# Kernel optimization log

Measured on AMD Instinct MI355X. Metric: run time of the kernel, lower is better.

## Reference

```python
import jax, jax.numpy as jnp
import numpy as np
from jax import lax

B, T_IN, T_OUT = 32, 384, 400
N_MEL, ENC, ATT_RNN, DEC_RNN, PRENET, ATT_DIM = 80, 512, 1024, 1024, 256, 128
LOC_F, LOC_K = 32, 31
NEG = -1e9  # stand-in for -inf score_mask_value (safe for softmax grad)


def setup_inputs() -> dict:
    key = jax.random.key(0)
    ks = jax.random.split(key, 20)
    g = lambda i, shape, s=0.02: jax.random.normal(ks[i], shape, dtype=jnp.float32) * s
    return {
        "memory": jax.random.normal(ks[0], (B, T_IN, ENC), dtype=jnp.float32),
        "decoder_inputs": jax.random.normal(ks[1], (B, N_MEL, T_OUT), dtype=jnp.float32),
        "memory_lengths": jax.random.randint(ks[2], (B,), T_IN // 2, T_IN + 1, dtype=jnp.int32),
        "prenet_w1": g(3, (PRENET, N_MEL)),
        "prenet_w2": g(4, (PRENET, PRENET)),
        "att_rnn_wih": g(5, (4 * ATT_RNN, PRENET + ENC)),
        "att_rnn_whh": g(6, (4 * ATT_RNN, ATT_RNN)),
        "att_rnn_bih": jnp.zeros((4 * ATT_RNN,), jnp.float32),
        "att_rnn_bhh": jnp.zeros((4 * ATT_RNN,), jnp.float32),
        "query_w": g(7, (ATT_DIM, ATT_RNN)),
        "memory_w": g(8, (ATT_DIM, ENC)),
        "v_w": g(9, (1, ATT_DIM)),
        "loc_conv_w": g(10, (LOC_F, 2, LOC_K)),
        "loc_dense_w": g(11, (ATT_DIM, LOC_F)),
        "dec_rnn_wih": g(12, (4 * DEC_RNN, ATT_RNN + ENC)),
        "dec_rnn_whh": g(13, (4 * DEC_RNN, DEC_RNN)),
        "dec_rnn_bih": jnp.zeros((4 * DEC_RNN,), jnp.float32),
        "dec_rnn_bhh": jnp.zeros((4 * DEC_RNN,), jnp.float32),
        "proj_w": g(14, (N_MEL, DEC_RNN + ENC)),
        "proj_b": jnp.zeros((N_MEL,), jnp.float32),
        "gate_w": g(15, (1, DEC_RNN + ENC)),
        "gate_b": jnp.zeros((1,), jnp.float32),
    }


def _lstm_cell(x, h, c, wih, whh, bih, bhh):
    gates = x @ wih.T + bih + h @ whh.T + bhh
    i, f, g, o = jnp.split(gates, 4, axis=-1)
    c2 = jax.nn.sigmoid(f) * c + jax.nn.sigmoid(i) * jnp.tanh(g)
    return jax.nn.sigmoid(o) * jnp.tanh(c2), c2


def reference(memory, decoder_inputs, memory_lengths, prenet_w1, prenet_w2,
              att_rnn_wih, att_rnn_whh, att_rnn_bih, att_rnn_bhh,
              query_w, memory_w, v_w, loc_conv_w, loc_dense_w,
              dec_rnn_wih, dec_rnn_whh, dec_rnn_bih, dec_rnn_bhh,
              proj_w, proj_b, gate_w, gate_b):
    pad = (LOC_K - 1) // 2
    pad_mask = jnp.arange(T_IN)[None, :] >= memory_lengths[:, None]  # (B, T_in), True = padded
    processed_memory = jnp.einsum('bte,ae->bta', memory, memory_w)  # (B, T_in, A)

    # parse_decoder_inputs + go frame: (T_out+1, B, n_mel)
    dec_in = jnp.concatenate([jnp.zeros((1, B, N_MEL), memory.dtype),
                              jnp.transpose(decoder_inputs, (2, 0, 1))], axis=0)
    # Prenet on whole teacher-forced sequence (eval: no dropout)
    pre = jax.nn.relu(jnp.einsum('tbm,pm->tbp', dec_in, prenet_w1))
    pre = jax.nn.relu(jnp.einsum('tbp,qp->tbq', pre, prenet_w2))  # (T_out+1, B, prenet)
    xs = pre[:-1]  # T_out decode steps

    def step(carry, x):
        ah, ac, dh, dc, aw, awc, ctx = carry
        # attention RNN
        ah, ac = _lstm_cell(jnp.concatenate([x, ctx], -1), ah, ac,
                            att_rnn_wih, att_rnn_whh, att_rnn_bih, att_rnn_bhh)
        # location-sensitive additive attention
        pq = (ah @ query_w.T)[:, None, :]  # (B, 1, A)
        cat = jnp.stack([aw, awc], axis=1)  # (B, 2, T_in)
        loc = lax.conv_general_dilated(cat, loc_conv_w, (1,), [(pad, pad)],
                                       dimension_numbers=('NCH', 'OIH', 'NCH'))  # (B, F, T_in)
        ploc = jnp.einsum('bft,af->bta', loc, loc_dense_w)  # (B, T_in, A)
        e = jnp.squeeze(jnp.tanh(pq + ploc + processed_memory) @ v_w.T, -1)  # (B, T_in)
        e = jnp.where(pad_mask, NEG, e)
        w = jax.nn.softmax(e, axis=1)
        ctx = jnp.einsum('bt,bte->be', w, memory)  # (B, enc)
        awc = awc + w
        # decoder RNN
        dh, dc = _lstm_cell(jnp.concatenate([ah, ctx], -1), dh, dc,
                            dec_rnn_wih, dec_rnn_whh, dec_rnn_bih, dec_rnn_bhh)
        hc = jnp.concatenate([dh, ctx], -1)  # (B, dec+enc)
        mel = hc @ proj_w.T + proj_b  # (B, n_mel)
        gate = hc @ gate_w.T + gate_b  # (B, 1)
        return (ah, ac, dh, dc, w, awc, ctx), (mel, gate, w)

    z = lambda d: jnp.zeros((B, d), memory.dtype)
    carry0 = (z(ATT_RNN), z(ATT_RNN), z(DEC_RNN), z(DEC_RNN),
              jnp.zeros((B, T_IN), memory.dtype), jnp.zeros((B, T_IN), memory.dtype), z(ENC))
    _, (mels, gates, aligns) = lax.scan(step, carry0, xs)
    mel_outputs = jnp.transpose(mels, (1, 2, 0))  # (B, n_mel, T_out)
    gate_outputs = jnp.transpose(jnp.squeeze(gates, -1), (1, 0))  # (B, T_out)
    alignments = jnp.transpose(aligns, (1, 0, 2))  # (B, T_out, T_in)
    return mel_outputs, gate_outputs, alignments
```

## Files before the change

kernel.cpp:

```cpp
#include <hip/hip_runtime.h>

typedef _Float16 h16;
typedef _Float16 half8 __attribute__((ext_vector_type(8)));
typedef float f32x4 __attribute__((ext_vector_type(4)));

#define NEGV -1000000000.0f
#define MFMA16(a,b,c) __builtin_amdgcn_mfma_f32_16x16x32_f16(a,b,c,0,0,0)

struct Params {
  const float *memory, *dec_in; const int *memlen;
  const float *w1, *w2;
  const float *awih, *awhh, *abih, *abhh;
  const float *qw, *mw, *vw, *lcw, *ldw;
  const float *dwih, *dwhh, *dbih, *dbhh;
  const float *pw, *pb, *gw, *gb;
  float *out, *ws;
};

constexpr long long XALLF_H = 0;
constexpr long long PMH_H   = 3276800;
constexpr long long PLB_H   = 4849664;
constexpr long long AWIHF_H = 6422528;
constexpr long long AWHHF_H = 9568256;
constexpr long long DWIHF_H = 13762560;
constexpr long long DWHHF_H = 20054016;
constexpr long long LCWF_H  = 24248320;
constexpr long long LDWF_H  = 24250368;
constexpr long long AHF_H   = 24254464;
constexpr long long DHF_H   = 24320000;
constexpr long long CTXF_H  = 24352768;
constexpr long long MEMF_H  = 24812544;
constexpr long long PWF_H   = 31104000;
constexpr long long QWF_H   = 31226880;
constexpr long long ZERO_F0 = 12127232;
constexpr long long AC_F    = 12184576;
constexpr long long DC_F    = 12217344;
constexpr long long AW_F    = 12250112;
constexpr long long AWC_F   = 12262400;
constexpr long long DPART_F = 12274688;
constexpr long long BAR_F   = 12405760;
constexpr int  ZERO_LEN = 278528;
constexpr unsigned NBLK = 512;
constexpr long long GATE0  = 1024000;
constexpr long long ALIGN0 = 1036800;

union SMem {
  float pmstage[12][512];
  struct { float x[5][80]; float l1[5][256]; } pre;
  struct { float red[16][2][16][17]; } g;
  struct { float awseg[2][128]; h16 im2[96][72]; h16 locT[96][32];
           unsigned p16[96][64]; } ploc;
  struct { float ah[1024]; float pq[128]; float pqp[8][128]; float vv[128];
           float e[384]; float w[384]; float red[32];
           float ctxred[4][256][2]; } row;
  struct { float hc[1536]; float mp[80][8]; float gacc; } mel;
};

__device__ __forceinline__ float sigf(float x){ return 1.0f/(1.0f+__expf(-x)); }
__device__ __forceinline__ float tanhfast(float x){ float e2 = __expf(2.0f*x); return 1.0f - 2.0f/(e2+1.0f); }

__device__ __forceinline__ float aldf(const float* p){
  return __hip_atomic_load(p, __ATOMIC_RELAXED, __HIP_MEMORY_SCOPE_AGENT);
}
__device__ __forceinline__ void astf(float* p, float v){
  __hip_atomic_store(p, v, __ATOMIC_RELAXED, __HIP_MEMORY_SCOPE_AGENT);
}
__device__ __forceinline__ unsigned long long aldu64(const h16* p){
  return __hip_atomic_load((const unsigned long long*)p, __ATOMIC_RELAXED, __HIP_MEMORY_SCOPE_AGENT);
}
__device__ __forceinline__ half8 ald16(const h16* p){
  union { unsigned long long q[2]; half8 v; } u;
  u.q[0] = __hip_atomic_load((const unsigned long long*)p,     __ATOMIC_RELAXED, __HIP_MEMORY_SCOPE_AGENT);
  u.q[1] = __hip_atomic_load(((const unsigned long long*)p)+1, __ATOMIC_RELAXED, __HIP_MEMORY_SCOPE_AGENT);
  return u.v;
}
__device__ __forceinline__ void asth(h16* p, float v){
  union { h16 h; unsigned short s; } u; u.h = (h16)v;
  __hip_atomic_store((unsigned short*)p, u.s, __ATOMIC_RELAXED, __HIP_MEMORY_SCOPE_AGENT);
}
__device__ __forceinline__ void astu32(unsigned* p, unsigned v){
  __hip_atomic_store(p, v, __ATOMIC_RELAXED, __HIP_MEMORY_SCOPE_AGENT);
}

__device__ __forceinline__ void gbar(unsigned* cnts, unsigned ep, bool full){
  __syncthreads();
  if (threadIdx.x == 0){
    if (full) __threadfence();
    __hip_atomic_fetch_add(&cnts[(blockIdx.x & 7)*64], 1u, __ATOMIC_RELEASE, __HIP_MEMORY_SCOPE_AGENT);
    const unsigned tgt = ep*NBLK;
    for (;;){
      unsigned s = 0;
      #pragma unroll
      for (int i = 0; i < 8; ++i)
        s += __hip_atomic_load(&cnts[i*64], __ATOMIC_RELAXED, __HIP_MEMORY_SCOPE_AGENT);
      if (s >= tgt) break;
      __builtin_amdgcn_s_sleep(4);
    }
    if (full) __threadfence();
  }
  __syncthreads();
}

__global__ void init_kernel(float* ws){
  unsigned* c = (unsigned*)(ws + BAR_F);
  if (threadIdx.x < 512) c[threadIdx.x] = 0u;
}

__global__ __launch_bounds__(1024, 8)
void decoder_kernel(Params P){
  __shared__ SMem sm;
  const int tid = threadIdx.x;
  const int bid = blockIdx.x;
  float* ws = P.ws;
  h16*   wsh = (h16*)ws;
  unsigned* bar = (unsigned*)(ws + BAR_F);
  unsigned ep = 0;

  const int lane = tid & 63, wv = tid >> 6;
  const int i16 = lane & 15, q = lane >> 4;

  {
    const long long gtid = (long long)bid*1024 + tid;
    const long long GS = 524288;
    for (long long i = gtid; i < ZERO_LEN; i += GS) ws[ZERO_F0 + i] = 0.f;
    for (long long i = gtid; i < 3145728; i += GS) wsh[AWIHF_H+i] = (h16)P.awih[i];
    for (long long i = gtid; i < 4194304; i += GS) wsh[AWHHF_H+i] = (h16)P.awhh[i];
    for (long long i = gtid; i < 6291456; i += GS) wsh[DWIHF_H+i] = (h16)P.dwih[i];
    for (long long i = gtid; i < 4194304; i += GS) wsh[DWHHF_H+i] = (h16)P.dwhh[i];
    for (long long i = gtid; i < 6291456; i += GS) wsh[MEMF_H+i] = (h16)P.memory[i];
    for (long long i = gtid; i < 122880; i += GS) wsh[PWF_H+i] = (h16)P.pw[i];
    for (long long i = gtid; i < 131072; i += GS) wsh[QWF_H+i] = (h16)P.qw[i];
    for (long long i = gtid; i < 2048; i += GS){
      int f = (int)(i >> 6), kk = (int)(i & 63), ch = kk >> 5, k = kk & 31;
      wsh[LCWF_H+i] = (k < 31) ? (h16)P.lcw[f*62 + ch*31 + k] : (h16)0.f;
    }
    for (long long i = gtid; i < 4096; i += GS) wsh[LDWF_H+i] = (h16)P.ldw[i];
  }
  {
    const int b = bid >> 4, part = bid & 15;
    for (int sub = 0; sub < 2; ++sub){
      const int t0 = part*24 + sub*12;
      __syncthreads();
      for (int i = tid; i < 1536; i += 1024){
        int row = i >> 7, c4 = (i & 127) << 2;
        *reinterpret_cast<float4*>(&sm.pmstage[row][c4]) =
          *reinterpret_cast<const float4*>(P.memory + ((long long)(b*384 + t0 + row))*512 + c4);
      }
      __syncthreads();
      if (tid < 512){
        const int a = tid & 127, th = tid >> 7;
        float acc[3] = {0,0,0};
        const float* mwr = P.mw + (long long)a*512;
        for (int e = 0; e < 512; ++e){
          float wvv = mwr[e];
          #pragma unroll
          for (int jj = 0; jj < 3; ++jj) acc[jj] += wvv*sm.pmstage[th*3+jj][e];
        }
        #pragma unroll
        for (int jj = 0; jj < 3; ++jj)
          wsh[PMH_H + ((long long)b*128 + a)*384 + t0 + th*3 + jj] = (h16)acc[jj];
      }
    }
  }
  {
    for (int batch = 0; batch < 5; ++batch){
      const int pbase = bid*25 + batch*5;
      __syncthreads();
      for (int i = tid; i < 400; i += 1024){
        int j = i/80, m = i%80;
        int p = pbase + j; int tq = p >> 5, bb = p & 31;
        float v = 0.f;
        if (tq > 0) v = P.dec_in[((long long)bb*80 + m)*400 + (tq-1)];
        sm.pre.x[j][m] = v;
      }
      __syncthreads();
      {
        float acc[5] = {0,0,0,0,0};
        if (tid < 256){
          const float* w1r = P.w1 + (long long)tid*80;
          for (int m = 0; m < 80; ++m){
            float wvv = w1r[m];
            #pragma unroll
            for (int j = 0; j < 5; ++j) acc[j] += wvv*sm.pre.x[j][m];
          }
        }
        __syncthreads();
        if (tid < 256){
          #pragma unroll
          for (int j = 0; j < 5; ++j) sm.pre.l1[j][tid] = fmaxf(acc[j], 0.f);
        }
      }
      __syncthreads();
      if (tid < 256){
        float acc[5] = {0,0,0,0,0};
        const float* w2r = P.w2 + (long long)tid*256;
        for (int pp = 0; pp < 256; ++pp){
          float wvv = w2r[pp];
          #pragma unroll
          for (int j = 0; j < 5; ++j) acc[j] += wvv*sm.pre.l1[j][pp];
        }
        #pragma unroll
        for (int j = 0; j < 5; ++j){
          int p = pbase + j; int tq = p >> 5, bb = p & 31;
          wsh[XALLF_H + ((long long)tq*32 + bb)*256 + tid] = (h16)fmaxf(acc[j], 0.f);
        }
      }
    }
  }
  gbar(bar, ++ep, true);

  for (int t = 0; t <= 400; ++t){
    const int cur = t & 1, prv = (t+1) & 1;

    if (bid < 256){
      if (t < 400){
        const int u0 = bid*4;
        const int n = ((i16 >> 2)*1024) + u0 + (i16 & 3);
        f32x4 acc0 = {0,0,0,0}, acc1 = {0,0,0,0};
        const long long prvO = (long long)prv*32768;
        const int s0 = (wv*56) >> 4, s1 = ((wv+1)*56) >> 4;
        for (int s = s0; s < s1; ++s){
          const int k0 = s*32;
          const h16* pA = (k0 < 768) ? wsh + AWIHF_H + (long long)n*768 + k0 + q*8
                                     : wsh + AWHHF_H + (long long)n*1024 + (k0-768) + q*8;
          half8 A = *(const half8*)pA;
          half8 B0, B1;
          if (k0 < 256){
            B0 = *(const half8*)(wsh + XALLF_H + ((long long)t*32 + i16)*256 + k0 + q*8);
            B1 = *(const half8*)(wsh + XALLF_H + ((long long)t*32 + 16 + i16)*256 + k0 + q*8);
          } else if (k0 < 768){
            B0 = ald16(wsh + CTXF_H + i16*512 + (k0-256) + q*8);
            B1 = ald16(wsh + CTXF_H + (16+i16)*512 + (k0-256) + q*8);
          } else {
            B0 = ald16(wsh + AHF_H + prvO + i16*1024 + (k0-768) + q*8);
            B1 = ald16(wsh + AHF_H + prvO + (16+i16)*1024 + (k0-768) + q*8);
          }
          acc0 = MFMA16(A, B0, acc0);
          acc1 = MFMA16(A, B1, acc1);
        }
        #pragma unroll
        for (int r = 0; r < 4; ++r){
          sm.g.red[wv][0][q*4+r][i16] = acc0[r];
          sm.g.red[wv][1][q*4+r][i16] = acc1[r];
        }
        __syncthreads();
        if (tid < 128){
          const int uu = tid >> 5, b = tid & 31;
          const int bt2 = b >> 4, c = b & 15;
          float g4[4];
          #pragma unroll
          for (int g = 0; g < 4; ++g){
            const int tr = g*4 + uu;
            float v = 0.f;
            #pragma unroll
            for (int w = 0; w < 16; ++w) v += sm.g.red[w][bt2][tr][c];
            const int ng = g*1024 + u0 + uu;
            g4[g] = v + P.abih[ng] + P.abhh[ng];
          }
          const long long idx = (long long)b*1024 + u0 + uu;
          float c2 = sigf(g4[1])*ws[AC_F + idx] + sigf(g4[0])*tanhfast(g4[2]);
          ws[AC_F + idx] = c2;
          asth(wsh + AHF_H + (long long)cur*32768 + idx, sigf(g4[3])*tanhfast(c2));
        }
      }
    } else if (bid < 384){
      if (t < 400){
        const int pb = bid - 256, b = pb >> 2, tbase = (pb & 3)*96;
        for (int i = tid; i < 252; i += 1024){
          int ch = i / 126, ix = i % 126;
          int pos = tbase - 15 + ix;
          float v = 0.f;
          if (pos >= 0 && pos < 384)
            v = aldf(ws + (ch ? AWC_F : AW_F) + b*384 + pos);
          sm.ploc.awseg[ch][ix] = v;
        }
        __syncthreads();
        for (int i = tid; i < 96*64; i += 1024){
          int tt = i >> 6, kk = i & 63, ch = kk >> 5, k = kk & 31;
          sm.ploc.im2[tt][kk] = (k < 31) ? (h16)sm.ploc.awseg[ch][tt + k] : (h16)0.f;
        }
        __syncthreads();
        {
          int tile = wv;
          if (tile < 12){
            int tT = tile % 6, tF = tile / 6;
            f32x4 a = {0,0,0,0};
            #pragma unroll
            for (int ks = 0; ks < 2; ++ks){
              half8 A = *(const half8*)&sm.ploc.im2[tT*16 + i16][ks*32 + q*8];
              half8 B = *(const half8*)(wsh + LCWF_H + (tF*16 + i16)*64 + ks*32 + q*8);
              a = MFMA16(A, B, a);
            }
            #pragma unroll
            for (int r = 0; r < 4; ++r)
              sm.ploc.locT[tT*16 + q*4 + r][tF*16 + i16] = (h16)a[r];
          }
        }
        __syncthreads();
        unsigned short* s16 = (unsigned short*)&sm.ploc.p16[0][0];
        #pragma unroll
        for (int p = 0; p < 3; ++p){
          int tile = wv + p*16;
          int tT = tile % 6, tA = tile / 6;
          half8 A = *(const half8*)&sm.ploc.locT[tT*16 + i16][q*8];
          half8 B = *(const half8*)(wsh + LDWF_H + (tA*16 + i16)*32 + q*8);
          f32x4 a = {0,0,0,0};
          a = MFMA16(A, B, a);
          int aa = tA*16 + i16;
          union { unsigned long long u; h16 h[4]; } pmu;
          pmu.u = *(const unsigned long long*)
              (wsh + PMH_H + ((long long)b*128 + aa)*384 + tbase + tT*16 + q*4);
          #pragma unroll
          for (int r = 0; r < 4; ++r){
            union { h16 h; unsigned short s; } cv;
            cv.h = (h16)(a[r] + (float)pmu.h[r]);
            s16[(tT*16 + q*4 + r)*128 + aa] = cv.s;
          }
        }
        __syncthreads();
        unsigned* plbu = (unsigned*)(wsh + PLB_H);
        for (int i = tid; i < 96*64; i += 1024){
          int tt = i >> 6, a2 = i & 63;
          astu32(plbu + ((long long)b*384 + tbase + tt)*64 + a2, sm.ploc.p16[tt][a2]);
        }
      }
    } else {
      if (t >= 1){
        const int u0 = (bid-384)*8;
        const int jt = wv & 1, kh = wv >> 1;
        const int n = ((i16 >> 2)*1024) + u0 + jt*4 + (i16 & 3);
        f32x4 acc0 = {0,0,0,0}, acc1 = {0,0,0,0};
        for (int s = kh*2; s < kh*2 + 2; ++s){
          const int k0 = s*32;
          half8 A = *(const half8*)(wsh + DWIHF_H + (long long)n*1536 + 1024 + k0 + q*8);
          half8 B0 = ald16(wsh + CTXF_H + i16*512 + k0 + q*8);
          half8 B1 = ald16(wsh + CTXF_H + (16+i16)*512 + k0 + q*8);
          acc0 = MFMA16(A, B0, acc0);
          acc1 = MFMA16(A, B1, acc1);
        }
        #pragma unroll
        for (int r = 0; r < 4; ++r){
          sm.g.red[wv][0][q*4+r][i16] = acc0[r];
          sm.g.red[wv][1][q*4+r][i16] = acc1[r];
        }
        __syncthreads();
        if (tid < 256){
          const int uu8 = tid >> 5, b = tid & 31;
          const int j2 = uu8 >> 2, uu = uu8 & 3;
          const int bt = b >> 4, c = b & 15;
          const int unit = u0 + j2*4 + uu;
          float g4[4];
          #pragma unroll
          for (int g = 0; g < 4; ++g){
            const int tr = g*4 + uu;
            const int ng = g*1024 + unit;
            float v = 0.f;
            #pragma unroll
            for (int k = 0; k < 8; ++k) v += sm.g.red[j2 + 2*k][bt][tr][c];
            g4[g] = v + aldf(ws + DPART_F + (long long)b*4096 + ng)
                  + P.dbih[ng] + P.dbhh[ng];
          }
          const long long idx = (long long)b*1024 + unit;
          float c2 = sigf(g4[1])*ws[DC_F + idx] + sigf(g4[0])*tanhfast(g4[2]);
          ws[DC_F + idx] = c2;
          asth(wsh + DHF_H + idx, sigf(g4[3])*tanhfast(c2));
        }
      }
    }
    gbar(bar, ++ep, false);

    if (bid < 32){
      if (t < 400){
        const int b = bid;
        const int len = P.memlen[b];
        if (tid < 256){
          union { unsigned long long u; h16 h[4]; } hu;
          hu.u = aldu64(wsh + AHF_H + (long long)cur*32768 + b*1024 + tid*4);
          #pragma unroll
          for (int j = 0; j < 4; ++j) sm.row.ah[tid*4+j] = (float)hu.h[j];
        }
        if (tid < 128) sm.row.vv[tid] = P.vw[tid];
        __syncthreads();
        {
          const int a = tid & 127, kh8 = tid >> 7;
          const h16* qr = wsh + QWF_H + (long long)a*1024 + kh8*128;
          const float* ahs = &sm.row.ah[kh8*128];
          float acc = 0.f;
          for (int k = 0; k < 128; k += 8){
            half8 wq = *(const half8*)(qr + k);
            acc += (float)wq[0]*ahs[k]   + (float)wq[1]*ahs[k+1]
                 + (float)wq[2]*ahs[k+2] + (float)wq[3]*ahs[k+3]
                 + (float)wq[4]*ahs[k+4] + (float)wq[5]*ahs[k+5]
                 + (float)wq[6]*ahs[k+6] + (float)wq[7]*ahs[k+7];
          }
          sm.row.pqp[kh8][a] = acc;
        }
        __syncthreads();
        if (tid < 128){
          float pqv = 0.f;
          #pragma unroll
          for (int k = 0; k < 8; ++k) pqv += sm.row.pqp[k][tid];
          sm.row.pq[tid] = pqv;
        }
        __syncthreads();
        {
          const int tt = tid;
          if (tt < 384){
            float acc;
            if (tt < len){
              acc = 0.f;
              const unsigned long long* plp = (const unsigned long long*)
                  (wsh + PLB_H + ((long long)b*384 + tt)*128);
              for (int a0 = 0; a0 < 32; ++a0){
                union { unsigned long long u; h16 h[4]; } hu;
                hu.u = __hip_atomic_load(plp + a0, __ATOMIC_RELAXED, __HIP_MEMORY_SCOPE_AGENT);
                #pragma unroll
                for (int j = 0; j < 4; ++j)
                  acc += sm.row.vv[a0*4+j]*tanhfast(sm.row.pq[a0*4+j] + (float)hu.h[j]);
              }
            } else acc = NEGV;
            sm.row.e[tt] = acc;
          }
        }
        __syncthreads();
        float m = NEGV;
        for (int tt = tid; tt < 384; tt += 1024) m = fmaxf(m, sm.row.e[tt]);
        for (int o = 32; o; o >>= 1) m = fmaxf(m, __shfl_xor(m, o, 64));
        if ((tid & 63) == 0) sm.row.red[tid >> 6] = m;
        __syncthreads();
        float mx = sm.row.red[0];
        #pragma unroll
        for (int w = 1; w < 16; ++w) mx = fmaxf(mx, sm.row.red[w]);
        float s = 0.f;
        for (int tt = tid; tt < 384; tt += 1024){
          float wvv = (tt < len) ? __expf(sm.row.e[tt] - mx) : 0.f;
          sm.row.w[tt] = wvv; s += wvv;
        }
        for (int o = 32; o; o >>= 1) s += __shfl_xor(s, o, 64);
        if ((tid & 63) == 0) sm.row.red[16 + (tid >> 6)] = s;
        __syncthreads();
        float ssum = sm.row.red[16];
        #pragma unroll
        for (int w = 1; w < 16; ++w) ssum += sm.row.red[16+w];
        const float inv = 1.f/ssum;
        for (int tt = tid; tt < 384; tt += 1024){
          float wvv = sm.row.w[tt]*inv;
          sm.row.w[tt] = wvv;
          astf(ws + AW_F + b*384 + tt, wvv);
          float oldc = aldf(ws + AWC_F + b*384 + tt);
          astf(ws + AWC_F + b*384 + tt, oldc + wvv);
          P.out[ALIGN0 + ((long long)b*400 + t)*384 + tt] = wvv;
        }
        __syncthreads();
        {
          const int col = tid & 255, rg = tid >> 8;
          const unsigned* mrow = (const unsigned*)(wsh + MEMF_H) + (long long)b*98304;
          float acc0 = 0.f, acc1 = 0.f;
          for (int t4 = rg*24; t4 < rg*24 + 24; ++t4){
            float4 w4 = *reinterpret_cast<const float4*>(&sm.row.w[t4*4]);
            const unsigned* m0 = mrow + t4*1024 + col;
            unsigned v0 = m0[0], v1 = m0[256], v2 = m0[512], v3 = m0[768];
            union { unsigned u; h16 h[2]; } d0, d1, d2, d3;
            d0.u = v0; d1.u = v1; d2.u = v2; d3.u = v3;
            acc0 += w4.x*(float)d0.h[0] + w4.y*(float)d1.h[0]
                  + w4.z*(float)d2.h[0] + w4.w*(float)d3.h[0];
            acc1 += w4.x*(float)d0.h[1] + w4.y*(float)d1.h[1]
                  + w4.z*(float)d2.h[1] + w4.w*(float)d3.h[1];
          }
          sm.row.ctxred[rg][col][0] = acc0;
          sm.row.ctxred[rg][col][1] = acc1;
          __syncthreads();
          if (tid < 256){
            union { h16 h[2]; unsigned u; } cv;
            cv.h[0] = (h16)(sm.row.ctxred[0][tid][0] + sm.row.ctxred[1][tid][0]
                          + sm.row.ctxred[2][tid][0] + sm.row.ctxred[3][tid][0]);
            cv.h[1] = (h16)(sm.row.ctxred[0][tid][1] + sm.row.ctxred[1][tid][1]
                          + sm.row.ctxred[2][tid][1] + sm.row.ctxred[3][tid][1]);
            astu32((unsigned*)(wsh + CTXF_H) + b*256 + tid, cv.u);
          }
        }
      }
    } else if (bid < 288){
      if (t < 400){
        const int n0 = (bid-32)*16;
        const int n = n0 + i16;
        f32x4 acc0 = {0,0,0,0}, acc1 = {0,0,0,0};
        const long long curO = (long long)cur*32768;
        for (int s = wv*4; s < wv*4 + 4; ++s){
          const int k0 = s*32;
          const h16* pA = (k0 < 1024) ? wsh + DWIHF_H + (long long)n*1536 + k0 + q*8
                                      : wsh + DWHHF_H + (long long)n*1024 + (k0-1024) + q*8;
          half8 A = *(const half8*)pA;
          half8 B0, B1;
          if (k0 < 1024){
            B0 = ald16(wsh + AHF_H + curO + i16*1024 + k0 + q*8);
            B1 = ald16(wsh + AHF_H + curO + (16+i16)*1024 + k0 + q*8);
          } else {
            B0 = ald16(wsh + DHF_H + i16*1024 + (k0-1024) + q*8);
            B1 = ald16(wsh + DHF_H + (16+i16)*1024 + (k0-1024) + q*8);
          }
          acc0 = MFMA16(A, B0, acc0);
          acc1 = MFMA16(A, B1, acc1);
        }
        #pragma unroll
        for (int r = 0; r < 4; ++r){
          sm.g.red[wv][0][q*4+r][i16] = acc0[r];
          sm.g.red[wv][1][q*4+r][i16] = acc1[r];
        }
        __syncthreads();
        if (tid < 256){
          const int r16 = tid & 15, c = tid >> 4;
          #pragma unroll
          for (int bt2 = 0; bt2 < 2; ++bt2){
            float v = 0.f;
            #pragma unroll
            for (int w = 0; w < 16; ++w) v += sm.g.red[w][bt2][r16][c];
            astf(ws + DPART_F + (long long)(bt2*16 + c)*4096 + n0 + r16, v);
          }
        }
      }
    } else if (bid < 320){
      if (t >= 1){
        const int b = bid - 288;
        for (int i = tid; i < 384; i += 1024){
          union { unsigned long long u; h16 h[4]; } hu;
          hu.u = (i < 256) ? aldu64(wsh + DHF_H + b*1024 + i*4)
                           : aldu64(wsh + CTXF_H + b*512 + (i-256)*4);
          #pragma unroll
          for (int j = 0; j < 4; ++j) sm.mel.hc[i*4+j] = (float)hu.h[j];
        }
        __syncthreads();
        if (tid < 640){
          const int r = tid >> 3, h8 = tid & 7;
          const h16* pr = wsh + PWF_H + (long long)r*1536 + h8*192;
          const float* hcp = &sm.mel.hc[h8*192];
          float acc = 0.f;
          for (int k = 0; k < 192; k += 8){
            half8 wq = *(const half8*)(pr + k);
            acc += (float)wq[0]*hcp[k]   + (float)wq[1]*hcp[k+1]
                 + (float)wq[2]*hcp[k+2] + (float)wq[3]*hcp[k+3]
                 + (float)wq[4]*hcp[k+4] + (float)wq[5]*hcp[k+5]
                 + (float)wq[6]*hcp[k+6] + (float)wq[7]*hcp[k+7];
          }
          sm.mel.mp[r][h8] = acc;
        } else if (tid >= 768 && tid < 832){
          const int l = tid - 768;
          const float* gp  = P.gw + l*24;
          const float* hcp = &sm.mel.hc[l*24];
          float acc = 0.f;
          #pragma unroll
          for (int k = 0; k < 24; ++k) acc += gp[k]*hcp[k];
          for (int o = 32; o; o >>= 1) acc += __shfl_xor(acc, o, 64);
          if (l == 0) sm.mel.gacc = acc;
        }
        __syncthreads();
        if (tid < 80){
          float v = P.pb[tid];
          #pragma unroll
          for (int k = 0; k < 8; ++k) v += sm.mel.mp[tid][k];
          P.out[((long long)b*80 + tid)*400 + (t-1)] = v;
        }
        if (tid == 80)
          P.out[GATE0 + (long long)b*400 + (t-1)] = sm.mel.gacc + P.gb[0];
      }
    }
    gbar(bar, ++ep, false);
  }
}

extern "C" void kernel_launch(void* const* d_in, const int* in_sizes, int n_in,
                              void* d_out, int out_size, void* d_ws, size_t ws_size,
                              hipStream_t stream) {
  (void)in_sizes; (void)n_in; (void)out_size; (void)ws_size;
  Params p;
  p.memory = (const float*)d_in[0];
  p.dec_in = (const float*)d_in[1];
  p.memlen = (const int*)d_in[2];
  p.w1   = (const float*)d_in[3];
  p.w2   = (const float*)d_in[4];
  p.awih = (const float*)d_in[5];
  p.awhh = (const float*)d_in[6];
  p.abih = (const float*)d_in[7];
  p.abhh = (const float*)d_in[8];
  p.qw   = (const float*)d_in[9];
  p.mw   = (const float*)d_in[10];
  p.vw   = (const float*)d_in[11];
  p.lcw  = (const float*)d_in[12];
  p.ldw  = (const float*)d_in[13];
  p.dwih = (const float*)d_in[14];
  p.dwhh = (const float*)d_in[15];
  p.dbih = (const float*)d_in[16];
  p.dbhh = (const float*)d_in[17];
  p.pw   = (const float*)d_in[18];
  p.pb   = (const float*)d_in[19];
  p.gw   = (const float*)d_in[20];
  p.gb   = (const float*)d_in[21];
  p.out  = (float*)d_out;
  p.ws   = (float*)d_ws;

  hipLaunchKernelGGL(init_kernel, dim3(1), dim3(512), 0, stream, p.ws);
  hipLaunchKernelGGL(decoder_kernel, dim3(512), dim3(1024), 0, stream, p);
}
```

Before: 44.18 ms.

## Halve blocks for attention and decoder LSTM gate GEMMs, two tiles per block

```diff
diff --git a/kernel.cpp b/kernel.cpp
--- a/kernel.cpp
+++ b/kernel.cpp
@@ -212,18 +212,20 @@
   for (int t = 0; t <= 400; ++t){
     const int cur = t & 1, prv = (t+1) & 1;
 
-    if (bid < 256){
+    if (bid < 128){
       if (t < 400){
-        const int u0 = bid*4;
+        const int u0 = bid*8;
         const int n = ((i16 >> 2)*1024) + u0 + (i16 & 3);
-        f32x4 acc0 = {0,0,0,0}, acc1 = {0,0,0,0};
+        f32x4 a00 = {0,0,0,0}, a01 = {0,0,0,0}, a10 = {0,0,0,0}, a11 = {0,0,0,0};
         const long long prvO = (long long)prv*32768;
         const int s0 = (wv*56) >> 4, s1 = ((wv+1)*56) >> 4;
         for (int s = s0; s < s1; ++s){
           const int k0 = s*32;
-          const h16* pA = (k0 < 768) ? wsh + AWIHF_H + (long long)n*768 + k0 + q*8
-                                     : wsh + AWHHF_H + (long long)n*1024 + (k0-768) + q*8;
-          half8 A = *(const half8*)pA;
+          const h16* base; long long stride4;
+          if (k0 < 768){ base = wsh + AWIHF_H + (long long)n*768 + k0 + q*8;  stride4 = 4ll*768; }
+          else         { base = wsh + AWHHF_H + (long long)n*1024 + (k0-768) + q*8; stride4 = 4ll*1024; }
+          half8 A0 = *(const half8*)base;
+          half8 A1 = *(const half8*)(base + stride4);
           half8 B0, B1;
           if (k0 < 256){
             B0 = *(const half8*)(wsh + XALLF_H + ((long long)t*32 + i16)*256 + k0 + q*8);
@@ -235,13 +237,15 @@
             B0 = ald16(wsh + AHF_H + prvO + i16*1024 + (k0-768) + q*8);
             B1 = ald16(wsh + AHF_H + prvO + (16+i16)*1024 + (k0-768) + q*8);
           }
-          acc0 = MFMA16(A, B0, acc0);
-          acc1 = MFMA16(A, B1, acc1);
+          a00 = MFMA16(A0, B0, a00);
+          a01 = MFMA16(A0, B1, a01);
+          a10 = MFMA16(A1, B0, a10);
+          a11 = MFMA16(A1, B1, a11);
         }
         #pragma unroll
         for (int r = 0; r < 4; ++r){
-          sm.g.red[wv][0][q*4+r][i16] = acc0[r];
-          sm.g.red[wv][1][q*4+r][i16] = acc1[r];
+          sm.g.red[wv][0][q*4+r][i16] = a00[r];
+          sm.g.red[wv][1][q*4+r][i16] = a01[r];
         }
         __syncthreads();
         if (tid < 128){
@@ -262,8 +266,33 @@
           ws[AC_F + idx] = c2;
           asth(wsh + AHF_H + (long long)cur*32768 + idx, sigf(g4[3])*tanhfast(c2));
         }
-      }
-    } else if (bid < 384){
+        __syncthreads();
+        #pragma unroll
+        for (int r = 0; r < 4; ++r){
+          sm.g.red[wv][0][q*4+r][i16] = a10[r];
+          sm.g.red[wv][1][q*4+r][i16] = a11[r];
+        }
+        __syncthreads();
+        if (tid < 128){
+          const int uu = tid >> 5, b = tid & 31;
+          const int bt2 = b >> 4, c = b & 15;
+          float g4[4];
+          #pragma unroll
+          for (int g = 0; g < 4; ++g){
+            const int tr = g*4 + uu;
+            float v = 0.f;
+            #pragma unroll
+            for (int w = 0; w < 16; ++w) v += sm.g.red[w][bt2][tr][c];
+            const int ng = g*1024 + u0 + 4 + uu;
+            g4[g] = v + P.abih[ng] + P.abhh[ng];
+          }
+          const long long idx = (long long)b*1024 + u0 + 4 + uu;
+          float c2 = sigf(g4[1])*ws[AC_F + idx] + sigf(g4[0])*tanhfast(g4[2]);
+          ws[AC_F + idx] = c2;
+          asth(wsh + AHF_H + (long long)cur*32768 + idx, sigf(g4[3])*tanhfast(c2));
+        }
+      }
+    } else if (bid >= 256 && bid < 384){
       if (t < 400){
         const int pb = bid - 256, b = pb >> 2, tbase = (pb & 3)*96;
         for (int i = tid; i < 252; i += 1024){
@@ -324,7 +353,7 @@
           astu32(plbu + ((long long)b*384 + tbase + tt)*64 + a2, sm.ploc.p16[tt][a2]);
         }
       }
-    } else {
+    } else if (bid >= 384){
       if (t >= 1){
         const int u0 = (bid-384)*8;
         const int jt = wv & 1, kh = wv >> 1;
@@ -480,17 +509,19 @@
           }
         }
       }
-    } else if (bid < 288){
+    } else if (bid < 160){
       if (t < 400){
-        const int n0 = (bid-32)*16;
+        const int n0 = (bid-32)*32;
         const int n = n0 + i16;
-        f32x4 acc0 = {0,0,0,0}, acc1 = {0,0,0,0};
+        f32x4 a00 = {0,0,0,0}, a01 = {0,0,0,0}, a10 = {0,0,0,0}, a11 = {0,0,0,0};
         const long long curO = (long long)cur*32768;
         for (int s = wv*4; s < wv*4 + 4; ++s){
           const int k0 = s*32;
-          const h16* pA = (k0 < 1024) ? wsh + DWIHF_H + (long long)n*1536 + k0 + q*8
-                                      : wsh + DWHHF_H + (long long)n*1024 + (k0-1024) + q*8;
-          half8 A = *(const half8*)pA;
+          const h16* base; long long stride16;
+          if (k0 < 1024){ base = wsh + DWIHF_H + (long long)n*1536 + k0 + q*8;        stride16 = 16ll*1536; }
+          else          { base = wsh + DWHHF_H + (long long)n*1024 + (k0-1024) + q*8; stride16 = 16ll*1024; }
+          half8 A0 = *(const half8*)base;
+          half8 A1 = *(const half8*)(base + stride16);
           half8 B0, B1;
           if (k0 < 1024){
             B0 = ald16(wsh + AHF_H + curO + i16*1024 + k0 + q*8);
@@ -499,13 +530,15 @@
             B0 = ald16(wsh + DHF_H + i16*1024 + (k0-1024) + q*8);
             B1 = ald16(wsh + DHF_H + (16+i16)*1024 + (k0-1024) + q*8);
           }
-          acc0 = MFMA16(A, B0, acc0);
-          acc1 = MFMA16(A, B1, acc1);
+          a00 = MFMA16(A0, B0, a00);
+          a01 = MFMA16(A0, B1, a01);
+          a10 = MFMA16(A1, B0, a10);
+          a11 = MFMA16(A1, B1, a11);
         }
         #pragma unroll
         for (int r = 0; r < 4; ++r){
-          sm.g.red[wv][0][q*4+r][i16] = acc0[r];
-          sm.g.red[wv][1][q*4+r][i16] = acc1[r];
+          sm.g.red[wv][0][q*4+r][i16] = a00[r];
+          sm.g.red[wv][1][q*4+r][i16] = a01[r];
         }
         __syncthreads();
         if (tid < 256){
@@ -518,8 +551,25 @@
             astf(ws + DPART_F + (long long)(bt2*16 + c)*4096 + n0 + r16, v);
           }
         }
-      }
-    } else if (bid < 320){
+        __syncthreads();
+        #pragma unroll
+        for (int r = 0; r < 4; ++r){
+          sm.g.red[wv][0][q*4+r][i16] = a10[r];
+          sm.g.red[wv][1][q*4+r][i16] = a11[r];
+        }
+        __syncthreads();
+        if (tid < 256){
+          const int r16 = tid & 15, c = tid >> 4;
+          #pragma unroll
+          for (int bt2 = 0; bt2 < 2; ++bt2){
+            float v = 0.f;
+            #pragma unroll
+            for (int w = 0; w < 16; ++w) v += sm.g.red[w][bt2][r16][c];
+            astf(ws + DPART_F + (long long)(bt2*16 + c)*4096 + n0 + 16 + r16, v);
+          }
+        }
+      }
+    } else if (bid >= 288 && bid < 320){
       if (t >= 1){
         const int b = bid - 288;
         for (int i = tid; i < 384; i += 1024){
```

After: 39.96 ms. 9.5% less time.
